# Optimization experiments

Measured on AMD Instinct MI355X. Metric: run time of the kernel, lower is better.

Reference implementation:

```python
import jax, jax.numpy as jnp
import numpy as np


def setup_inputs() -> dict:
    key = jax.random.key(0)
    ks = jax.random.split(key, 8)
    B, T, D, R, V = 2, 2048, 2048, 32, 32000
    hidden = jax.random.normal(ks[0], (B, T, D), dtype=jnp.float32)
    targets = jax.random.randint(ks[1], (B, T), 0, V, dtype=jnp.int32)
    lm_head_weight = jax.random.normal(ks[2], (V, D), dtype=jnp.float32) * 0.02
    delta_A = jax.random.normal(ks[3], (D, R), dtype=jnp.float32) * 0.01
    delta_B = jax.random.normal(ks[4], (R, D), dtype=jnp.float32) * 0.01
    decay_gate_W = jax.random.normal(ks[5], (1, D), dtype=jnp.float32) * 0.02
    decay_gate_b = jnp.full((1,), 2.0, dtype=jnp.float32)  # nn.init.constant_(bias, 2.0)
    log_step_size = jnp.full((1,), -6.9, dtype=jnp.float32)
    return {
        "hidden": hidden,
        "targets": targets,
        "lm_head_weight": lm_head_weight,
        "delta_A": delta_A,
        "delta_B": delta_B,
        "decay_gate_W": decay_gate_W,
        "decay_gate_b": decay_gate_b,
        "log_step_size": log_step_size,
    }


def reference(hidden, targets, lm_head_weight, delta_A, delta_B,
              decay_gate_W, decay_gate_b, log_step_size):
    """One InPlaceTTT interaction for a single TTT layer:
    1. Titans-style decay gating: alpha = sigmoid(decay_gate(mean_BT(hidden))),
       deltas scaled by alpha.
    2. apply_delta: out = hidden + (hidden @ B^T) @ A^T.
    3. ttt_step: analytic gradient of next-token CE loss (via frozen lm_head)
       w.r.t. the low-rank deltas; one SGD step of size exp(log_step_size).
    Returns (out, A_new, B_new).
    """
    Bsz, T, D = hidden.shape
    N = Bsz * T
    h = hidden.reshape(N, D)

    # --- decay gate ---
    pooled = h.mean(axis=0)                                  # [D]
    alpha = jax.nn.sigmoid(pooled @ decay_gate_W[0] + decay_gate_b[0])  # scalar
    A = delta_A * alpha                                      # [D, R]
    Bm = delta_B * alpha                                     # [R, D]

    # --- apply delta ---
    z = h @ Bm.T                                             # [N, R]
    o = h + z @ A.T                                          # [N, D]
    out = o.reshape(Bsz, T, D)

    # --- TTT step: analytic CE gradient through frozen lm_head ---
    logits = o @ lm_head_weight.T                            # [N, V]
    probs = jax.nn.softmax(logits, axis=-1)                  # [N, V]
    # dL/do = (probs - onehot(targets)) @ W / N, computed without one-hot
    tgt = targets.reshape(N)
    G = (probs @ lm_head_weight - lm_head_weight[tgt]) / N   # [N, D]
    gA = G.T @ z                                             # [D, R]
    gB = (G @ A).T @ h                                       # [R, D]

    step = jnp.exp(log_step_size[0])
    A_new = A - step * gA
    B_new = Bm - step * gB
    return out, A_new, B_new
```

## Files before the change

### kernel.cpp

```cpp
#include <hip/hip_runtime.h>
#include <hip/hip_bf16.h>


typedef __bf16 bf16;
typedef __attribute__((ext_vector_type(8))) __bf16 bf16x8;
typedef __attribute__((ext_vector_type(4))) __bf16 bf16x4;
typedef __attribute__((ext_vector_type(4))) float f32x4;

#define DEV static __device__ __forceinline__

static constexpr int Tn = 2048, Dm = 2048, Rr = 32, Vv = 32000;
static constexpr int Nn = 2 * Tn;
static constexpr float INV_N = 1.0f / (float)Nn;
static constexpr int RED_CHUNKS = 16;
static constexpr int RED_NI = Nn / RED_CHUNKS;

DEV void gload_lds16(const void* g, void* l) {
  __builtin_amdgcn_global_load_lds(
      (const __attribute__((address_space(1))) unsigned int*)(unsigned long long)g,
      (__attribute__((address_space(3))) unsigned int*)(unsigned int)(unsigned long long)l,
      16, 0, 0);
}

__global__ __launch_bounds__(512, 2)
void k_gemm1(const bf16* __restrict__ A, const bf16* __restrict__ Bm, int K,
             bf16* __restrict__ Pout, float* __restrict__ lsum) {
  __shared__ __attribute__((aligned(16))) char smem[131072];
  const int t = threadIdx.x;
  const int lane = t & 63;
  const int fr = lane & 15;
  const int fq = lane >> 4;
  const int w = t >> 6, wm = w >> 2, wn = w & 3;
  const int m0 = blockIdx.x * 256, n0 = blockIdx.y * 256;

  const int sr = t >> 3;
  const int sb = t & 7;
  const int gbk = sb ^ (sr & 7);
  const bf16* aS = A + (size_t)(m0 + sr) * K + gbk * 8;
  const bf16* bS = Bm + (size_t)(n0 + sr) * K + gbk * 8;
  char* aD = smem + sr * 128 + sb * 16;
  char* bD = smem + 32768 + sr * 128 + sb * 16;

  auto STAGE = [&](int db, int kt) {
    const bf16* ga = aS + (size_t)kt * 64;
    const bf16* gb2 = bS + (size_t)kt * 64;
    char* la = aD + db * 65536;
    char* lb = bD + db * 65536;
#pragma unroll
    for (int c = 0; c < 4; ++c) {
      gload_lds16(ga + (size_t)c * 64 * K, la + c * 8192);
      gload_lds16(gb2 + (size_t)c * 64 * K, lb + c * 8192);
    }
  };

  f32x4 acc[8][4] = {};

  STAGE(0, 0);
  STAGE(1, 1);
  asm volatile("s_waitcnt vmcnt(8)" ::: "memory");
  __builtin_amdgcn_s_barrier();

  const int NT = K >> 6;
  int db = 0;
  for (int kt = 0; kt < NT; ++kt) {
    const char* bufA = smem + db * 65536;
    const char* bufB = bufA + 32768;
#pragma unroll
    for (int kk = 0; kk < 2; ++kk) {
      const int bp = ((kk * 4 + fq) ^ (fr & 7)) * 16;
      bf16x8 af[8], bfr[4];
#pragma unroll
      for (int i = 0; i < 8; ++i)
        af[i] = *(const bf16x8*)(bufA + (wm * 128 + i * 16 + fr) * 128 + bp);
#pragma unroll
      for (int j = 0; j < 4; ++j)
        bfr[j] = *(const bf16x8*)(bufB + (wn * 64 + j * 16 + fr) * 128 + bp);
      __builtin_amdgcn_s_setprio(1);
#pragma unroll
      for (int i = 0; i < 8; ++i)
#pragma unroll
        for (int j = 0; j < 4; ++j)
          acc[i][j] = __builtin_amdgcn_mfma_f32_16x16x32_bf16(af[i], bfr[j], acc[i][j], 0, 0, 0);
      __builtin_amdgcn_s_setprio(0);
    }
    __builtin_amdgcn_s_barrier();
    if (kt + 2 < NT) {
      STAGE(db, kt + 2);
      asm volatile("s_waitcnt vmcnt(8)" ::: "memory");
      __builtin_amdgcn_s_barrier();
    } else if (kt + 1 < NT) {
      asm volatile("s_waitcnt vmcnt(0)" ::: "memory");
      __builtin_amdgcn_s_barrier();
    }
    db ^= 1;
  }

  __builtin_amdgcn_s_barrier();
  bf16* tile = (bf16*)smem;
#pragma unroll
  for (int p = 0; p < 2; ++p) {
    if (wm == p) {
#pragma unroll
      for (int i = 0; i < 8; ++i)
#pragma unroll
        for (int j = 0; j < 4; ++j)
#pragma unroll
          for (int rg = 0; rg < 4; ++rg)
            tile[(i * 16 + fq * 4 + rg) * 264 + wn * 64 + j * 16 + fr] =
                (bf16)__expf(acc[i][j][rg]);
    }
    __builtin_amdgcn_s_barrier();
    {
      const int r = t >> 2, cb = (t & 3) * 64;
      const bf16* src = tile + r * 264 + cb;
      bf16* dst = Pout + (size_t)(m0 + p * 128 + r) * Vv + n0 + cb;
      float s = 0.f;
#pragma unroll
      for (int q = 0; q < 8; ++q) {
        bf16x8 v = *(const bf16x8*)&src[q * 8];
        *(bf16x8*)&dst[q * 8] = v;
#pragma unroll
        for (int e = 0; e < 8; ++e) s += (float)v[e];
      }
      s += __shfl_xor(s, 1);
      s += __shfl_xor(s, 2);
      if ((t & 3) == 0) atomicAdd(&lsum[m0 + p * 128 + r], s);
    }
    __builtin_amdgcn_s_barrier();
  }
}

template<int EPI, bool SW>
__global__ __launch_bounds__(256)
void k_gemm(const bf16* __restrict__ A, const bf16* __restrict__ B, int K,
            bf16* __restrict__ Pout, float* __restrict__ lsum,
            const float* __restrict__ Wf,
            const int* __restrict__ tgt, float* __restrict__ Gout)
{
  const int m0 = (SW ? blockIdx.y : blockIdx.x) * 128;
  const int n0 = (SW ? blockIdx.x : blockIdx.y) * 128;
  const int t = threadIdx.x;
  const int lane = t & 63;
  const int w = t >> 6;
  const int wr = (w >> 1) * 64;
  const int wc = (w & 1) * 64;

  __shared__ bf16 smem[2 * 128 * 64];
  bf16* As = smem;
  bf16* Bs = smem + 128 * 64;

  f32x4 acc[4][4] = {};

  const bf16* a0 = A + (size_t)(m0 + (t >> 3)) * K + (t & 7) * 8;
  const bf16* b0 = B + (size_t)(n0 + (t >> 3)) * K + (t & 7) * 8;
  bf16* asl = As + t * 8;
  bf16* bsl = Bs + t * 8;

  for (int kt = 0; kt < K; kt += 64) {
#pragma unroll
    for (int j = 0; j < 4; ++j) {
      gload_lds16(a0 + (size_t)j * 32 * K + kt, asl + j * 2048);
      gload_lds16(b0 + (size_t)j * 32 * K + kt, bsl + j * 2048);
    }
    __syncthreads();
#pragma unroll
    for (int kk = 0; kk < 2; ++kk) {
      bf16x8 af[4], bff[4];
#pragma unroll
      for (int i = 0; i < 4; ++i)
        af[i] = *(const bf16x8*)&As[(wr + i * 16 + (lane & 15)) * 64 + kk * 32 + (lane >> 4) * 8];
#pragma unroll
      for (int i = 0; i < 4; ++i)
        bff[i] = *(const bf16x8*)&Bs[(wc + i * 16 + (lane & 15)) * 64 + kk * 32 + (lane >> 4) * 8];
#pragma unroll
      for (int i = 0; i < 4; ++i)
#pragma unroll
        for (int j = 0; j < 4; ++j)
          acc[i][j] = __builtin_amdgcn_mfma_f32_16x16x32_bf16(af[i], bff[j], acc[i][j], 0, 0, 0);
    }
    __syncthreads();
  }

  const int cl = lane & 15;
  const int rl4 = (lane >> 4) * 4;

#pragma unroll
  for (int i = 0; i < 4; ++i) {
    const int rbase = m0 + wr + i * 16 + rl4;
    float rl[4]; int tg[4];
#pragma unroll
    for (int rg = 0; rg < 4; ++rg) {
      rl[rg] = INV_N / lsum[rbase + rg];
      tg[rg] = tgt[rbase + rg];
    }
#pragma unroll
    for (int j = 0; j < 4; ++j) {
      const int c = n0 + wc + j * 16 + cl;
#pragma unroll
      for (int rg = 0; rg < 4; ++rg)
        Gout[(size_t)(rbase + rg) * Dm + c] =
            acc[i][j][rg] * rl[rg] - Wf[(size_t)tg[rg] * Dm + c] * INV_N;
    }
  }
}

__global__ __launch_bounds__(256) void k_zero(float* __restrict__ p, int n) {
  const int i = blockIdx.x * 256 + threadIdx.x;
  if (i < n) p[i] = 0.f;
}

__global__ __launch_bounds__(256) void k_colmean(const float* __restrict__ h,
                                                 float* __restrict__ pooled) {
  const int t = threadIdx.x;
  const int d = blockIdx.x * 32 + (t & 31);
  const int rp = t >> 5;
  float s = 0.f;
  for (int r = rp; r < Nn; r += 8) s += h[(size_t)r * Dm + d];
  __shared__ float red[8][32];
  red[rp][t & 31] = s;
  __syncthreads();
  if (t < 32) {
    float tot = 0.f;
#pragma unroll
    for (int j = 0; j < 8; ++j) tot += red[j][t];
    pooled[blockIdx.x * 32 + t] = tot;
  }
}

__global__ __launch_bounds__(256)
void k_scal(const float* __restrict__ pooled, const float* __restrict__ gw,
            const float* __restrict__ gb, const float* __restrict__ lss,
            float* __restrict__ scal) {
  const int t = threadIdx.x;
  float s = 0.f;
  for (int d = t; d < Dm; d += 256) s += pooled[d] * gw[d];
  __shared__ float red[256];
  red[t] = s; __syncthreads();
  for (int off = 128; off > 0; off >>= 1) {
    if (t < off) red[t] += red[t + off];
    __syncthreads();
  }
  if (t == 0) {
    const float x = red[0] * INV_N + gb[0];
    scal[0] = 1.0f / (1.0f + expf(-x));
    scal[1] = expf(lss[0]);
  }
}

__global__ __launch_bounds__(256)
void k_convW(const float* __restrict__ W, bf16* __restrict__ Wb,
             bf16* __restrict__ WbT) {
  __shared__ bf16 tile[64][72];
  const int t = threadIdx.x;
  const int v0 = blockIdx.x * 64, d0 = blockIdx.y * 64;
#pragma unroll
  for (int p = 0; p < 4; ++p) {
    const int v = (t >> 4) + p * 16, dc = (t & 15) * 4;
    float4 f = *(const float4*)&W[(size_t)(v0 + v) * Dm + d0 + dc];
    bf16 b0 = (bf16)f.x, b1 = (bf16)f.y, b2 = (bf16)f.z, b3 = (bf16)f.w;
    bf16x4 pk; pk[0] = b0; pk[1] = b1; pk[2] = b2; pk[3] = b3;
    *(bf16x4*)&Wb[(size_t)(v0 + v) * Dm + d0 + dc] = pk;
    tile[v][dc] = b0; tile[v][dc + 1] = b1; tile[v][dc + 2] = b2; tile[v][dc + 3] = b3;
  }
  __syncthreads();
  const int dr = t >> 2, c0 = (t & 3) * 16;
  bf16x8 x0, x1;
#pragma unroll
  for (int i = 0; i < 8; ++i) { x0[i] = tile[c0 + i][dr]; x1[i] = tile[c0 + 8 + i][dr]; }
  bf16* dst = WbT + (size_t)(d0 + dr) * Vv + v0 + c0;
  *(bf16x8*)&dst[0] = x0;
  *(bf16x8*)&dst[8] = x1;
}

__global__ __launch_bounds__(256)
void k_z(const float* __restrict__ h, const float* __restrict__ dB,
         const float* __restrict__ scal, float* __restrict__ z) {
  __shared__ float hs[16][132];
  const int t = threadIdx.x;
  const int n0 = blockIdx.x * 16;
  const int row = t >> 4;
  const int rp = (t & 15) * 2;
  float a0 = 0.f, a1 = 0.f;
  for (int dc = 0; dc < Dm; dc += 128) {
#pragma unroll
    for (int j = 0; j < 2; ++j) {
      const int e = (t + j * 256) * 4;
      const int r = e >> 7, c = e & 127;
      *(float4*)&hs[r][c] = *(const float4*)&h[(size_t)(n0 + r) * Dm + dc + c];
    }
    __syncthreads();
    const float* b0p = dB + (size_t)rp * Dm + dc;
    const float* b1p = dB + (size_t)(rp + 1) * Dm + dc;
#pragma unroll 4
    for (int d4 = 0; d4 < 128; d4 += 4) {
      float4 hv = *(const float4*)&hs[row][d4];
      float4 b0 = *(const float4*)&b0p[d4];
      float4 b1 = *(const float4*)&b1p[d4];
      a0 += hv.x * b0.x + hv.y * b0.y + hv.z * b0.z + hv.w * b0.w;
      a1 += hv.x * b1.x + hv.y * b1.y + hv.z * b1.z + hv.w * b1.w;
    }
    __syncthreads();
  }
  const float alpha = scal[0];
  z[(size_t)(n0 + row) * Rr + rp] = a0 * alpha;
  z[(size_t)(n0 + row) * Rr + rp + 1] = a1 * alpha;
}

__global__ __launch_bounds__(256)
void k_o(const float* __restrict__ h, const float* __restrict__ dA,
         const float* __restrict__ z, const float* __restrict__ scal,
         float* __restrict__ out, bf16* __restrict__ ob) {
  __shared__ float zs[64][36];
  __shared__ float sa[128][36];
  const int t = threadIdx.x;
  const int n0 = blockIdx.x * 64, d0 = blockIdx.y * 128;
  const float alpha = scal[0];
#pragma unroll
  for (int j = 0; j < 2; ++j) {
    const int e = (t + j * 256) * 4;
    *(float4*)&zs[e >> 5][e & 31] = *(const float4*)&z[(size_t)n0 * Rr + e];
  }
#pragma unroll
  for (int j = 0; j < 4; ++j) {
    const int e = (t + j * 256) * 4;
    const int r = e >> 5, c = e & 31;
    float4 f = *(const float4*)&dA[(size_t)(d0 + r) * Rr + c];
    f.x *= alpha; f.y *= alpha; f.z *= alpha; f.w *= alpha;
    *(float4*)&sa[r][c] = f;
  }
  __syncthreads();
  const int row = t >> 2, dq = (t & 3) * 32;
  float zr[32];
#pragma unroll
  for (int r = 0; r < 32; ++r) zr[r] = zs[row][r];
  const float* hrow = h + (size_t)(n0 + row) * Dm + d0 + dq;
  float* orow = out + (size_t)(n0 + row) * Dm + d0 + dq;
  bf16* obrow = ob + (size_t)(n0 + row) * Dm + d0 + dq;
#pragma unroll
  for (int d4 = 0; d4 < 32; d4 += 4) {
    float4 hv = *(const float4*)&hrow[d4];
    float o4[4];
#pragma unroll
    for (int k = 0; k < 4; ++k) {
      float s = 0.f;
#pragma unroll
      for (int r4 = 0; r4 < 32; r4 += 4) {
        float4 sv = *(const float4*)&sa[dq + d4 + k][r4];
        s += zr[r4] * sv.x + zr[r4 + 1] * sv.y + zr[r4 + 2] * sv.z + zr[r4 + 3] * sv.w;
      }
      o4[k] = (&hv.x)[k] + s;
    }
    float4 ov; ov.x = o4[0]; ov.y = o4[1]; ov.z = o4[2]; ov.w = o4[3];
    *(float4*)&orow[d4] = ov;
    bf16x4 bv; bv[0] = (bf16)o4[0]; bv[1] = (bf16)o4[1]; bv[2] = (bf16)o4[2]; bv[3] = (bf16)o4[3];
    *(bf16x4*)&obrow[d4] = bv;
  }
}

__global__ __launch_bounds__(256)
void k_u(const float* __restrict__ G, const float* __restrict__ dA,
         const float* __restrict__ scal, float* __restrict__ u) {
  __shared__ float gr[Dm];
  const int n = blockIdx.x, t = threadIdx.x;
#pragma unroll
  for (int j = 0; j < 2; ++j)
    *(float4*)&gr[(t + j * 256) * 4] = *(const float4*)&G[(size_t)n * Dm + (t + j * 256) * 4];
  __syncthreads();
  const int r = t & 31, jp = t >> 5;
  float s = 0.f;
  for (int i = 0; i < Dm / 8; ++i) {
    const int d = jp + i * 8;
    s += gr[d] * dA[(size_t)d * Rr + r];
  }
  __shared__ float red[8][32];
  red[jp][r] = s;
  __syncthreads();
  if (t < 32) {
    float tot = 0.f;
#pragma unroll
    for (int j = 0; j < 8; ++j) tot += red[j][t];
    u[(size_t)n * Rr + t] = tot * scal[0];
  }
}

template<bool TR>
__global__ __launch_bounds__(256)
void k_red_nr(const float* __restrict__ X, const float* __restrict__ Y,
              float* __restrict__ part) {
  __shared__ float ylds[RED_NI][32];
  const int t = threadIdx.x;
  const int dg = (t & 31) * 4;
  const int rg = (t >> 5) * 4;
  const int d0 = blockIdx.x * 128;
  const int n0 = blockIdx.y * RED_NI;
#pragma unroll
  for (int j = 0; j < 8; ++j) {
    const int e = (t + j * 256) * 4;
    *(float4*)&ylds[e >> 5][e & 31] = *(const float4*)&Y[(size_t)n0 * Rr + e];
  }
  __syncthreads();
  float acc[4][4] = {};
#pragma unroll 4
  for (int ni = 0; ni < RED_NI; ++ni) {
    float4 x4 = *(const float4*)&X[(size_t)(n0 + ni) * Dm + d0 + dg];
#pragma unroll
    for (int q = 0; q < 4; ++q) {
      const float yv = ylds[ni][rg + q];
      acc[0][q] += x4.x * yv;
      acc[1][q] += x4.y * yv;
      acc[2][q] += x4.z * yv;
      acc[3][q] += x4.w * yv;
    }
  }
  float* dst = part + (size_t)blockIdx.y * (Dm * Rr);
#pragma unroll
  for (int p = 0; p < 4; ++p)
#pragma unroll
    for (int q = 0; q < 4; ++q) {
      const int d = d0 + dg + p, r = rg + q;
      dst[TR ? (size_t)r * Dm + d : (size_t)d * Rr + r] = acc[p][q];
    }
}

__global__ __launch_bounds__(256)
void k_final(const float* __restrict__ dA, const float* __restrict__ dB,
             const float* __restrict__ gAp, const float* __restrict__ gBp,
             const float* __restrict__ scal,
             float* __restrict__ outA, float* __restrict__ outB) {
  const int i = blockIdx.x * 256 + threadIdx.x;
  const float alpha = scal[0], step = scal[1];
  float sa = 0.f, sb = 0.f;
#pragma unroll
  for (int j = 0; j < RED_CHUNKS; ++j) {
    sa += gAp[(size_t)j * Dm * Rr + i];
    sb += gBp[(size_t)j * Dm * Rr + i];
  }
  outA[i] = alpha * dA[i] - step * sa;
  outB[i] = alpha * dB[i] - step * sb;
}

extern "C" void kernel_launch(void* const* d_in, const int* in_sizes, int n_in,
                              void* d_out, int out_size, void* d_ws, size_t ws_size,
                              hipStream_t stream) {
  const float* hidden = (const float*)d_in[0];
  const int* targets  = (const int*)d_in[1];
  const float* W      = (const float*)d_in[2];
  const float* dA     = (const float*)d_in[3];
  const float* dB     = (const float*)d_in[4];
  const float* gw     = (const float*)d_in[5];
  const float* gb     = (const float*)d_in[6];
  const float* lss    = (const float*)d_in[7];

  auto al = [](size_t b) { return (b + 255) & ~(size_t)255; };
  const size_t szWb  = al((size_t)Vv * Dm * 2);
  const size_t szWbT = al((size_t)Dm * Vv * 2);
  const size_t szOb  = al((size_t)Nn * Dm * 2);
  const size_t szG   = al((size_t)Nn * Dm * 4);
  const size_t szZ   = al((size_t)Nn * Rr * 4);
  const size_t szU   = szZ;
  const size_t szLs  = al((size_t)Nn * 4);
  const size_t szPl  = al((size_t)Dm * 4);
  const size_t szSc  = al(256);
  const size_t szPart= al((size_t)RED_CHUNKS * Dm * Rr * 4);
  const size_t fixed = szWb + szWbT + szOb + szG + szZ + szU + szLs + szPl + szSc + 2 * szPart;

  int Nc = Nn;
  while (Nc > 256 && fixed + al((size_t)Nc * Vv * 2) > ws_size) Nc >>= 1;
  if (fixed + al((size_t)Nc * Vv * 2) > ws_size) return;

  char* base = (char*)d_ws;
  size_t off = 0;
  auto alloc = [&](size_t bytes) -> void* { void* q = base + off; off += al(bytes); return q; };
  bf16*  Wb    = (bf16*)alloc((size_t)Vv * Dm * 2);
  bf16*  WbT   = (bf16*)alloc((size_t)Dm * Vv * 2);
  bf16*  ob    = (bf16*)alloc((size_t)Nn * Dm * 2);
  float* G     = (float*)alloc((size_t)Nn * Dm * 4);
  float* z     = (float*)alloc((size_t)Nn * Rr * 4);
  float* u     = (float*)alloc((size_t)Nn * Rr * 4);
  float* lsum  = (float*)alloc((size_t)Nn * 4);
  float* pooled= (float*)alloc((size_t)Dm * 4);
  float* scal  = (float*)alloc(256);
  float* gAp   = (float*)alloc((size_t)RED_CHUNKS * Dm * Rr * 4);
  float* gBp   = (float*)alloc((size_t)RED_CHUNKS * Dm * Rr * 4);
  bf16*  P     = (bf16*)alloc((size_t)Nc * Vv * 2);

  float* out  = (float*)d_out;
  float* outA = out + (size_t)Nn * Dm;
  float* outB = outA + (size_t)Dm * Rr;

  k_colmean<<<Dm / 32, 256, 0, stream>>>(hidden, pooled);
  k_scal<<<1, 256, 0, stream>>>(pooled, gw, gb, lss, scal);
  k_convW<<<dim3(Vv / 64, Dm / 64), 256, 0, stream>>>(W, Wb, WbT);
  k_zero<<<(Nn + 255) / 256, 256, 0, stream>>>(lsum, Nn);
  k_z<<<Nn / 16, 256, 0, stream>>>(hidden, dB, scal, z);
  k_o<<<dim3(Nn / 64, Dm / 128), 256, 0, stream>>>(hidden, dA, z, scal, out, ob);

  for (int ns = 0; ns < Nn; ns += Nc) {
    k_gemm1<<<dim3(Nc / 256, Vv / 256), 512, 0, stream>>>(
        ob + (size_t)ns * Dm, Wb, Dm, P, lsum + ns);
    k_gemm<1, true><<<dim3(Dm / 128, Nc / 128), 256, 0, stream>>>(
        P, WbT, Vv, nullptr, lsum + ns, W, targets + ns, G + (size_t)ns * Dm);
  }

  k_u<<<Nn, 256, 0, stream>>>(G, dA, scal, u);
  k_red_nr<false><<<dim3(Dm / 128, RED_CHUNKS), 256, 0, stream>>>(G, z, gAp);
  k_red_nr<true><<<dim3(Dm / 128, RED_CHUNKS), 256, 0, stream>>>(hidden, u, gBp);
  k_final<<<Dm * Rr / 256, 256, 0, stream>>>(dA, dB, gAp, gBp, scal, outA, outB);
}
```

Baseline: 2.406 ms.

## Chunk vocabulary dimension and add double-buffered 256x128 second GEMM

The vocabulary is split into chunks of VC columns, so the bf16 probability buffer P is Nn x VC and can stay small enough to be L2/MALL resident between the two GEMMs. G is accumulated across chunks, and the softmax normalisation and target subtraction are applied only on the last chunk. The second GEMM is rewritten as a 512-thread kernel with 256x128 tiles, double-buffered global-to-LDS loads, a swizzled LDS layout and setprio around the MFMAs. In exchange, G is read and written once per chunk, which adds fp32 traffic and kernel launches.

```diff
diff --git a/kernel.cpp b/kernel.cpp
--- a/kernel.cpp
+++ b/kernel.cpp
@@ -24,7 +24,7 @@
 
 __global__ __launch_bounds__(512, 2)
 void k_gemm1(const bf16* __restrict__ A, const bf16* __restrict__ Bm, int K,
-             bf16* __restrict__ Pout, float* __restrict__ lsum) {
+             bf16* __restrict__ Pout, int Pld, float* __restrict__ lsum) {
   __shared__ __attribute__((aligned(16))) char smem[131072];
   const int t = threadIdx.x;
   const int lane = t & 63;
@@ -113,7 +113,7 @@
     {
       const int r = t >> 2, cb = (t & 3) * 64;
       const bf16* src = tile + r * 264 + cb;
-      bf16* dst = Pout + (size_t)(m0 + p * 128 + r) * Vv + n0 + cb;
+      bf16* dst = Pout + (size_t)(m0 + p * 128 + r) * Pld + n0 + cb;
       float s = 0.f;
 #pragma unroll
       for (int q = 0; q < 8; ++q) {
@@ -130,76 +130,100 @@
   }
 }
 
-template<int EPI, bool SW>
-__global__ __launch_bounds__(256)
-void k_gemm(const bf16* __restrict__ A, const bf16* __restrict__ B, int K,
-            bf16* __restrict__ Pout, float* __restrict__ lsum,
-            const float* __restrict__ Wf,
-            const int* __restrict__ tgt, float* __restrict__ Gout)
-{
-  const int m0 = (SW ? blockIdx.y : blockIdx.x) * 128;
-  const int n0 = (SW ? blockIdx.x : blockIdx.y) * 128;
+template<int MODE>
+__global__ __launch_bounds__(512, 2)
+void k_gemm2(const bf16* __restrict__ A, int K,
+             const bf16* __restrict__ Bw, int Bld,
+             float* __restrict__ G, const float* __restrict__ lsum,
+             const float* __restrict__ Wf, const int* __restrict__ tgt) {
+  __shared__ __attribute__((aligned(16))) char smem[98304];
   const int t = threadIdx.x;
   const int lane = t & 63;
-  const int w = t >> 6;
-  const int wr = (w >> 1) * 64;
-  const int wc = (w & 1) * 64;
-
-  __shared__ bf16 smem[2 * 128 * 64];
-  bf16* As = smem;
-  bf16* Bs = smem + 128 * 64;
+  const int fr = lane & 15, fq = lane >> 4;
+  const int w = t >> 6, wm = w >> 1, wn = w & 1;
+  const int m0 = blockIdx.x * 256, d0 = blockIdx.y * 128;
+
+  const int sr = t >> 3, sb = t & 7;
+  const int gbk = sb ^ (sr & 7);
+  const bf16* aS = A + (size_t)(m0 + sr) * K + gbk * 8;
+  const bf16* bS = Bw + (size_t)(d0 + sr) * Bld + gbk * 8;
+  char* aD = smem + sr * 128 + sb * 16;
+  char* bD = smem + 32768 + sr * 128 + sb * 16;
+
+  auto STAGE = [&](int db, int kt) {
+    char* la = aD + db * 49152;
+    char* lb = bD + db * 49152;
+#pragma unroll
+    for (int c = 0; c < 4; ++c)
+      gload_lds16(aS + (size_t)kt * 64 + (size_t)c * 64 * K, la + c * 8192);
+#pragma unroll
+    for (int c = 0; c < 2; ++c)
+      gload_lds16(bS + (size_t)kt * 64 + (size_t)c * 64 * Bld, lb + c * 8192);
+  };
 
   f32x4 acc[4][4] = {};
-
-  const bf16* a0 = A + (size_t)(m0 + (t >> 3)) * K + (t & 7) * 8;
-  const bf16* b0 = B + (size_t)(n0 + (t >> 3)) * K + (t & 7) * 8;
-  bf16* asl = As + t * 8;
-  bf16* bsl = Bs + t * 8;
-
-  for (int kt = 0; kt < K; kt += 64) {
+  STAGE(0, 0);
+  STAGE(1, 1);
+  asm volatile("s_waitcnt vmcnt(6)" ::: "memory");
+  __builtin_amdgcn_s_barrier();
+
+  const int NT = K >> 6;
+  int db = 0;
+  for (int kt = 0; kt < NT; ++kt) {
+    const char* bufA = smem + db * 49152;
+    const char* bufB = bufA + 32768;
+#pragma unroll
+    for (int kk = 0; kk < 2; ++kk) {
+      const int bp = ((kk * 4 + fq) ^ (fr & 7)) * 16;
+      bf16x8 af[4], bf4[4];
+#pragma unroll
+      for (int i = 0; i < 4; ++i)
+        af[i] = *(const bf16x8*)(bufA + (wm * 64 + i * 16 + fr) * 128 + bp);
+#pragma unroll
+      for (int j = 0; j < 4; ++j)
+        bf4[j] = *(const bf16x8*)(bufB + (wn * 64 + j * 16 + fr) * 128 + bp);
+      __builtin_amdgcn_s_setprio(1);
+#pragma unroll
+      for (int i = 0; i < 4; ++i)
+#pragma unroll
+        for (int j = 0; j < 4; ++j)
+          acc[i][j] = __builtin_amdgcn_mfma_f32_16x16x32_bf16(af[i], bf4[j], acc[i][j], 0, 0, 0);
+      __builtin_amdgcn_s_setprio(0);
+    }
+    __builtin_amdgcn_s_barrier();
+    if (kt + 2 < NT) {
+      STAGE(db, kt + 2);
+      asm volatile("s_waitcnt vmcnt(6)" ::: "memory");
+      __builtin_amdgcn_s_barrier();
+    } else if (kt + 1 < NT) {
+      asm volatile("s_waitcnt vmcnt(0)" ::: "memory");
+      __builtin_amdgcn_s_barrier();
+    }
+    db ^= 1;
+  }
+
+#pragma unroll
+  for (int i = 0; i < 4; ++i) {
+    const int m4 = m0 + wm * 64 + i * 16 + fq * 4;
+    float rl[4]; int tg[4];
+    if (MODE & 2) {
+#pragma unroll
+      for (int rg = 0; rg < 4; ++rg) {
+        rl[rg] = INV_N / lsum[m4 + rg];
+        tg[rg] = tgt[m4 + rg];
+      }
+    }
 #pragma unroll
     for (int j = 0; j < 4; ++j) {
-      gload_lds16(a0 + (size_t)j * 32 * K + kt, asl + j * 2048);
-      gload_lds16(b0 + (size_t)j * 32 * K + kt, bsl + j * 2048);
-    }
-    __syncthreads();
-#pragma unroll
-    for (int kk = 0; kk < 2; ++kk) {
-      bf16x8 af[4], bff[4];
-#pragma unroll
-      for (int i = 0; i < 4; ++i)
-        af[i] = *(const bf16x8*)&As[(wr + i * 16 + (lane & 15)) * 64 + kk * 32 + (lane >> 4) * 8];
-#pragma unroll
-      for (int i = 0; i < 4; ++i)
-        bff[i] = *(const bf16x8*)&Bs[(wc + i * 16 + (lane & 15)) * 64 + kk * 32 + (lane >> 4) * 8];
-#pragma unroll
-      for (int i = 0; i < 4; ++i)
-#pragma unroll
-        for (int j = 0; j < 4; ++j)
-          acc[i][j] = __builtin_amdgcn_mfma_f32_16x16x32_bf16(af[i], bff[j], acc[i][j], 0, 0, 0);
-    }
-    __syncthreads();
-  }
-
-  const int cl = lane & 15;
-  const int rl4 = (lane >> 4) * 4;
-
-#pragma unroll
-  for (int i = 0; i < 4; ++i) {
-    const int rbase = m0 + wr + i * 16 + rl4;
-    float rl[4]; int tg[4];
-#pragma unroll
-    for (int rg = 0; rg < 4; ++rg) {
-      rl[rg] = INV_N / lsum[rbase + rg];
-      tg[rg] = tgt[rbase + rg];
-    }
-#pragma unroll
-    for (int j = 0; j < 4; ++j) {
-      const int c = n0 + wc + j * 16 + cl;
-#pragma unroll
-      for (int rg = 0; rg < 4; ++rg)
-        Gout[(size_t)(rbase + rg) * Dm + c] =
-            acc[i][j][rg] * rl[rg] - Wf[(size_t)tg[rg] * Dm + c] * INV_N;
+      const int d = d0 + wn * 64 + j * 16 + fr;
+#pragma unroll
+      for (int rg = 0; rg < 4; ++rg) {
+        float v = acc[i][j][rg];
+        float* gp = &G[(size_t)(m4 + rg) * Dm + d];
+        if (MODE & 1) v += *gp;
+        if (MODE & 2) v = v * rl[rg] - Wf[(size_t)tg[rg] * Dm + d] * INV_N;
+        *gp = v;
+      }
     }
   }
 }
@@ -452,21 +476,14 @@
   const float* lss    = (const float*)d_in[7];
 
   auto al = [](size_t b) { return (b + 255) & ~(size_t)255; };
-  const size_t szWb  = al((size_t)Vv * Dm * 2);
-  const size_t szWbT = al((size_t)Dm * Vv * 2);
-  const size_t szOb  = al((size_t)Nn * Dm * 2);
-  const size_t szG   = al((size_t)Nn * Dm * 4);
-  const size_t szZ   = al((size_t)Nn * Rr * 4);
-  const size_t szU   = szZ;
-  const size_t szLs  = al((size_t)Nn * 4);
-  const size_t szPl  = al((size_t)Dm * 4);
-  const size_t szSc  = al(256);
-  const size_t szPart= al((size_t)RED_CHUNKS * Dm * Rr * 4);
-  const size_t fixed = szWb + szWbT + szOb + szG + szZ + szU + szLs + szPl + szSc + 2 * szPart;
-
-  int Nc = Nn;
-  while (Nc > 256 && fixed + al((size_t)Nc * Vv * 2) > ws_size) Nc >>= 1;
-  if (fixed + al((size_t)Nc * Vv * 2) > ws_size) return;
+  const size_t fixed =
+      al((size_t)Vv * Dm * 2) + al((size_t)Dm * Vv * 2) + al((size_t)Nn * Dm * 2) +
+      al((size_t)Nn * Dm * 4) + 2 * al((size_t)Nn * Rr * 4) + al((size_t)Nn * 4) +
+      al((size_t)Dm * 4) + al((size_t)256) + 2 * al((size_t)RED_CHUNKS * Dm * Rr * 4);
+
+  int VC = 6400;
+  while (VC > 1600 && fixed + al((size_t)Nn * VC * 2) > ws_size) VC >>= 1;
+  if (fixed + al((size_t)Nn * VC * 2) > ws_size) return;
 
   char* base = (char*)d_ws;
   size_t off = 0;
@@ -482,7 +499,7 @@
   float* scal  = (float*)alloc(256);
   float* gAp   = (float*)alloc((size_t)RED_CHUNKS * Dm * Rr * 4);
   float* gBp   = (float*)alloc((size_t)RED_CHUNKS * Dm * Rr * 4);
-  bf16*  P     = (bf16*)alloc((size_t)Nc * Vv * 2);
+  bf16*  P     = (bf16*)alloc((size_t)Nn * VC * 2);
 
   float* out  = (float*)d_out;
   float* outA = out + (size_t)Nn * Dm;
@@ -495,11 +512,21 @@
   k_z<<<Nn / 16, 256, 0, stream>>>(hidden, dB, scal, z);
   k_o<<<dim3(Nn / 64, Dm / 128), 256, 0, stream>>>(hidden, dA, z, scal, out, ob);
 
-  for (int ns = 0; ns < Nn; ns += Nc) {
-    k_gemm1<<<dim3(Nc / 256, Vv / 256), 512, 0, stream>>>(
-        ob + (size_t)ns * Dm, Wb, Dm, P, lsum + ns);
-    k_gemm<1, true><<<dim3(Dm / 128, Nc / 128), 256, 0, stream>>>(
-        P, WbT, Vv, nullptr, lsum + ns, W, targets + ns, G + (size_t)ns * Dm);
+  const int nch = Vv / VC;
+  for (int c = 0; c < nch; ++c) {
+    k_gemm1<<<dim3(Nn / 256, VC / 256), 512, 0, stream>>>(
+        ob, Wb + (size_t)c * VC * Dm, Dm, P, VC, lsum);
+    const int mode = (c > 0 ? 1 : 0) | (c == nch - 1 ? 2 : 0);
+    const dim3 g2(Nn / 256, Dm / 128);
+    const bf16* Bw = WbT + (size_t)c * VC;
+    if (mode == 0)
+      k_gemm2<0><<<g2, 512, 0, stream>>>(P, VC, Bw, Vv, G, lsum, W, targets);
+    else if (mode == 1)
+      k_gemm2<1><<<g2, 512, 0, stream>>>(P, VC, Bw, Vv, G, lsum, W, targets);
+    else if (mode == 2)
+      k_gemm2<2><<<g2, 512, 0, stream>>>(P, VC, Bw, Vv, G, lsum, W, targets);
+    else
+      k_gemm2<3><<<g2, 512, 0, stream>>>(P, VC, Bw, Vv, G, lsum, W, targets);
   }
 
   k_u<<<Nn, 256, 0, stream>>>(G, dA, scal, u);
```

After: 2.309 ms. -4.0%, faster.
